# Kernel tuning notes

Measured on AMD Instinct MI355X. Metric: run time of the kernel, lower is better.

## Reference

```python
import jax, jax.numpy as jnp
import numpy as np


def setup_inputs() -> dict:
    key = jax.random.key(0)
    k1, k2 = jax.random.split(key)
    B, T, F, H = 64, 512, 512, 1024
    x = jax.random.normal(k1, (B, T, F), dtype=jnp.float32)
    W = jax.random.normal(k2, (F + H, H), dtype=jnp.float32) * (1.0 / np.sqrt(F + H))
    b = jnp.zeros((H,), dtype=jnp.float32)
    return {"x": x, "W": W, "b": b}


def reference(x, W, b):
    # Vanilla tanh RNN: state_t = tanh([x_t, state_{t-1}] @ W + b); return last state.
    B, T, F = x.shape
    H = b.shape[0]
    Wx, Wh = W[:F], W[F:]  # split weight: input part [F,H], recurrent part [H,H]
    # Precompute input projections for all timesteps in one big GEMM.
    xproj = jnp.einsum('btf,fh->bth', x, Wx) + b  # [B,T,H]

    def step(state, xp_t):
        state = jnp.tanh(xp_t + state @ Wh)
        return state, None

    state0 = jnp.zeros((B, H), dtype=x.dtype)
    final_state, _ = jax.lax.scan(step, state0, jnp.swapaxes(xproj, 0, 1))
    return final_state
```

## Files before the change

kernel.cpp:

```cpp
#include <hip/hip_runtime.h>


typedef _Float16 f16;
typedef _Float16 f16x8 __attribute__((ext_vector_type(8)));
typedef _Float16 f16x4 __attribute__((ext_vector_type(4)));
typedef float f32x4 __attribute__((ext_vector_type(4)));

#define B_  64
#define T_  512
#define F_  512
#define H_  1024

#define XPH_OFF  0ull
#define WXT_OFF  67108864ull
#define WHT_OFF  68157440ull
#define SBUF_OFF 70254592ull
#define BAR_OFF  70516736ull
#define WS_NEED  70518784ull

__global__ __launch_bounds__(256) void k_prep(const float* __restrict__ W,
                                              f16* __restrict__ WxT,
                                              f16* __restrict__ WhT) {
  __shared__ float tile[32][33];
  const int tid = threadIdx.x;
  const int kt = blockIdx.x >> 5;
  const int ht = blockIdx.x & 31;
#pragma unroll
  for (int p = 0; p < 4; ++p) {
    int kr = p * 8 + (tid >> 5);
    tile[kr][tid & 31] = W[(size_t)(kt * 32 + kr) * 1024 + ht * 32 + (tid & 31)];
  }
  __syncthreads();
  const int hl = tid >> 3;
  const int kq = tid & 7;
  f16x4 v;
#pragma unroll
  for (int j = 0; j < 4; ++j) v[j] = (f16)tile[kq * 4 + j][hl];
  const int h = ht * 32 + hl;
  const int kg = kt * 32 + kq * 4;
  if (kg < 512) *(f16x4*)(WxT + (size_t)h * 512 + kg) = v;
  else          *(f16x4*)(WhT + (size_t)h * 1024 + (kg - 512)) = v;
}

__global__ __launch_bounds__(256) void k_xproj(const float* __restrict__ x,
                                               const f16* __restrict__ WxT,
                                               const float* __restrict__ bias,
                                               f16* __restrict__ xph) {
  __shared__ __align__(16) unsigned char Al[65536];
  __shared__ __align__(16) unsigned char Bl[65536];
  const int tid = threadIdx.x;
  const int l = tid & 63, w = tid >> 6;
  const int lane15 = l & 15, sub = l >> 4;
  const int m0 = blockIdx.x * 64;
  const int bidx = m0 >> 9;
  const int t0 = m0 & 511;

  {
    const int r = tid >> 2, qq = tid & 3;
    const float* xs = x + (size_t)(m0 + r) * 512;
#pragma unroll
    for (int i = 0; i < 16; ++i) {
      int s = qq * 16 + i;
      int c = s ^ (r & 7);
      const float4 f0 = *(const float4*)(xs + c * 8);
      const float4 f1 = *(const float4*)(xs + c * 8 + 4);
      f16x8 v;
      v[0] = (f16)f0.x; v[1] = (f16)f0.y; v[2] = (f16)f0.z; v[3] = (f16)f0.w;
      v[4] = (f16)f1.x; v[5] = (f16)f1.y; v[6] = (f16)f1.z; v[7] = (f16)f1.w;
      *(f16x8*)(Al + r * 1024 + s * 16) = v;
    }
  }

  const int mh = (w >> 1) * 32, nh = (w & 1) * 32;
  const int rA0 = mh + lane15, rA1 = mh + 16 + lane15;
  const int rB0 = nh + lane15, rB1 = nh + 16 + lane15;

  for (int nb = 0; nb < 16; ++nb) {
    const int n0 = nb * 64;
    __syncthreads();
    {
      const int r = tid >> 2, qq = tid & 3;
      const f16* bs = WxT + (size_t)(n0 + r) * 512;
#pragma unroll
      for (int i = 0; i < 16; ++i) {
        int s = qq * 16 + i;
        int c = s ^ (r & 7);
        f16x8 v = *(const f16x8*)(bs + c * 8);
        *(f16x8*)(Bl + r * 1024 + s * 16) = v;
      }
    }
    __syncthreads();
    f32x4 acc00 = {0.f,0.f,0.f,0.f}, acc01 = {0.f,0.f,0.f,0.f};
    f32x4 acc10 = {0.f,0.f,0.f,0.f}, acc11 = {0.f,0.f,0.f,0.f};
#pragma unroll
    for (int kk = 0; kk < 16; ++kk) {
      const int s = kk * 4 + sub;
      f16x8 a0 = *(const f16x8*)(Al + rA0 * 1024 + ((s ^ (rA0 & 7)) << 4));
      f16x8 a1 = *(const f16x8*)(Al + rA1 * 1024 + ((s ^ (rA1 & 7)) << 4));
      f16x8 b0 = *(const f16x8*)(Bl + rB0 * 1024 + ((s ^ (rB0 & 7)) << 4));
      f16x8 b1 = *(const f16x8*)(Bl + rB1 * 1024 + ((s ^ (rB1 & 7)) << 4));
      acc00 = __builtin_amdgcn_mfma_f32_16x16x32_f16(a0, b0, acc00, 0, 0, 0);
      acc01 = __builtin_amdgcn_mfma_f32_16x16x32_f16(a0, b1, acc01, 0, 0, 0);
      acc10 = __builtin_amdgcn_mfma_f32_16x16x32_f16(a1, b0, acc10, 0, 0, 0);
      acc11 = __builtin_amdgcn_mfma_f32_16x16x32_f16(a1, b1, acc11, 0, 0, 0);
    }
    const float bv0 = bias[n0 + nh + lane15];
    const float bv1 = bias[n0 + nh + 16 + lane15];
#pragma unroll
    for (int j = 0; j < 4; ++j) {
      const int r0 = mh + sub * 4 + j;
      const int r1 = mh + 16 + sub * 4 + j;
      const size_t row0 = (size_t)(t0 + r0) * 64 + bidx;
      const size_t row1 = (size_t)(t0 + r1) * 64 + bidx;
      xph[row0 * 1024 + n0 + nh + lane15]      = (f16)(acc00[j] + bv0);
      xph[row0 * 1024 + n0 + nh + 16 + lane15] = (f16)(acc01[j] + bv1);
      xph[row1 * 1024 + n0 + nh + lane15]      = (f16)(acc10[j] + bv0);
      xph[row1 * 1024 + n0 + nh + 16 + lane15] = (f16)(acc11[j] + bv1);
    }
  }
}

__global__ __launch_bounds__(256, 1) void k_rnn(const f16* __restrict__ xph,
                                                const f16* __restrict__ WhT,
                                                f16* sbuf, unsigned* bar,
                                                float* __restrict__ out) {
  __shared__ __align__(16) unsigned char lds[32768 + 2176];
  unsigned char* stL  = lds;
  unsigned char* tbuf = lds + 32768;
  const int tid = threadIdx.x;
  const int l = tid & 63, w = tid >> 6;
  const int lane15 = l & 15, sub = l >> 4;
  const int bid = blockIdx.x;
  const int group = (bid & 7) >> 1;
  const int slice = (bid >> 3) * 2 + (bid & 1);

  const int colL = slice * 64 + w * 16 + lane15;
  f16x8 breg[32];
  {
    const f16* src = WhT + (size_t)colL * 1024 + sub * 8;
#pragma unroll
    for (int kk = 0; kk < 32; ++kk) breg[kk] = *(const f16x8*)(src + kk * 32);
  }
  const int rA = lane15, xA = rA & 7;
  const unsigned char* stLb = stL + rA * 2048;

  const int p = tid >> 4, q = tid & 15;
  unsigned* myflag   = bar + (group * 16 + slice) * 8;
  unsigned* pollflag = bar + (group * 16 + p) * 8;
  const bool do_poll = (p != slice);

  for (int t = 0; t < T_; ++t) {
    const char* ib = (const char*)sbuf + (size_t)(t & 1) * 131072 + group * 32768;
    char*       ob = (char*)sbuf + (size_t)((t + 1) & 1) * 131072 + group * 32768;

    float xpv[4];
#pragma unroll
    for (int j = 0; j < 4; ++j)
      xpv[j] = (float)xph[(size_t)(t * 64 + group * 16 + sub * 4 + j) * 1024 + colL];

    if (t > 0 && do_poll) {
      while (__hip_atomic_load(pollflag, __ATOMIC_RELAXED,
                               __HIP_MEMORY_SCOPE_AGENT) < (unsigned)t) {}
    }
    {
      unsigned long long tmp[16];
      const char* src = ib + p * 128 + q * 8;
#pragma unroll
      for (int i = 0; i < 16; ++i)
        tmp[i] = __hip_atomic_load((const unsigned long long*)(src + i * 2048),
                                   __ATOMIC_RELAXED, __HIP_MEMORY_SCOPE_AGENT);
#pragma unroll
      for (int i = 0; i < 16; ++i)
        *(unsigned long long*)(stL + i * 2048 + p * 128 + q * 8) = tmp[i];
    }
    __syncthreads();

    f32x4 acc0 = {0.f,0.f,0.f,0.f}, acc1 = {0.f,0.f,0.f,0.f};
    f32x4 acc2 = {0.f,0.f,0.f,0.f}, acc3 = {0.f,0.f,0.f,0.f};
#pragma unroll
    for (int kk = 0; kk < 32; kk += 4) {
      f16x8 a0 = *(const f16x8*)(stLb + ((((kk + 0) * 4 + sub) ^ xA) << 4));
      f16x8 a1 = *(const f16x8*)(stLb + ((((kk + 1) * 4 + sub) ^ xA) << 4));
      f16x8 a2 = *(const f16x8*)(stLb + ((((kk + 2) * 4 + sub) ^ xA) << 4));
      f16x8 a3 = *(const f16x8*)(stLb + ((((kk + 3) * 4 + sub) ^ xA) << 4));
      acc0 = __builtin_amdgcn_mfma_f32_16x16x32_f16(a0, breg[kk + 0], acc0, 0, 0, 0);
      acc1 = __builtin_amdgcn_mfma_f32_16x16x32_f16(a1, breg[kk + 1], acc1, 0, 0, 0);
      acc2 = __builtin_amdgcn_mfma_f32_16x16x32_f16(a2, breg[kk + 2], acc2, 0, 0, 0);
      acc3 = __builtin_amdgcn_mfma_f32_16x16x32_f16(a3, breg[kk + 3], acc3, 0, 0, 0);
    }
    float rv[4];
#pragma unroll
    for (int j = 0; j < 4; ++j)
      rv[j] = acc0[j] + acc1[j] + acc2[j] + acc3[j] + xpv[j];

    if (t == T_ - 1) {
#pragma unroll
      for (int j = 0; j < 4; ++j)
        out[(size_t)(group * 16 + sub * 4 + j) * 1024 + colL] = tanhf(rv[j]);
      break;
    }

#pragma unroll
    for (int j = 0; j < 4; ++j) {
      f16 hv = (f16)tanhf(rv[j]);
      *(f16*)(tbuf + (sub * 4 + j) * 136 + (w * 16 + lane15) * 2) = hv;
    }
    asm volatile("s_waitcnt lgkmcnt(0)" ::: "memory");
    const int rr = lane15, cg = sub;
    unsigned long long packed =
        *(const unsigned long long*)(tbuf + rr * 136 + (w * 16 + cg * 4) * 2);
    const int c0 = slice * 64 + w * 16 + cg * 4;
    const int byteoff = rr * 2048 + (((c0 >> 3) ^ (rr & 7)) << 4) + (c0 & 7) * 2;
    __hip_atomic_store((unsigned long long*)(ob + byteoff), packed,
                       __ATOMIC_RELAXED, __HIP_MEMORY_SCOPE_AGENT);

    asm volatile("s_waitcnt vmcnt(0)" ::: "memory");
    __syncthreads();
    if (tid == 0)
      __hip_atomic_store(myflag, (unsigned)(t + 1),
                         __ATOMIC_RELAXED, __HIP_MEMORY_SCOPE_AGENT);
  }
}

extern "C" void kernel_launch(void* const* d_in, const int* in_sizes, int n_in,
                              void* d_out, int out_size, void* d_ws, size_t ws_size,
                              hipStream_t stream) {
  const float* x    = (const float*)d_in[0];
  const float* W    = (const float*)d_in[1];
  const float* bias = (const float*)d_in[2];
  float* out = (float*)d_out;
  char* w = (char*)d_ws;

  f16* xph = (f16*)(w + XPH_OFF);
  f16* WxT = (f16*)(w + WXT_OFF);
  f16* WhT = (f16*)(w + WHT_OFF);
  f16* sbuf = (f16*)(w + SBUF_OFF);
  unsigned* bar = (unsigned*)(w + BAR_OFF);

  hipMemsetAsync(w + SBUF_OFF, 0, 262144 + 2048, stream);

  k_prep<<<dim3(48 * 32), dim3(256), 0, stream>>>(W, WxT, WhT);
  k_xproj<<<dim3(512), dim3(256), 0, stream>>>(x, WxT, bias, xph);
  k_rnn<<<dim3(64), dim3(256), 0, stream>>>(xph, WhT, sbuf, bar, out);
}
```

Measured before the change: 1.808 ms.

## Replace flag barrier with per-element step tags in the recurrent state exchange

Each fp16 hidden value is now stored in a 32-bit word together with the step index, so consumers poll the data words themselves instead of waiting on per-slice flags. This removes the vmcnt wait, the extra __syncthreads and the separate flag store and poll that sat on each timestep's critical path. The cost is that the exchanged state doubles in size, and there is extra unpacking and tag-checking work per load. A register pin on the weight fragments is also added.

```diff
diff --git a/kernel.cpp b/kernel.cpp
--- a/kernel.cpp
+++ b/kernel.cpp
@@ -5,6 +5,8 @@
 typedef _Float16 f16x8 __attribute__((ext_vector_type(8)));
 typedef _Float16 f16x4 __attribute__((ext_vector_type(4)));
 typedef float f32x4 __attribute__((ext_vector_type(4)));
+typedef unsigned long long u64;
+typedef unsigned u32;
 
 #define B_  64
 #define T_  512
@@ -15,8 +17,10 @@
 #define WXT_OFF  67108864ull
 #define WHT_OFF  68157440ull
 #define SBUF_OFF 70254592ull
-#define BAR_OFF  70516736ull
-#define WS_NEED  70518784ull
+#define WS_NEED  70778880ull
+
+#define ALD(p)    __hip_atomic_load((const u64*)(p), __ATOMIC_RELAXED, __HIP_MEMORY_SCOPE_AGENT)
+#define AST(p, v) __hip_atomic_store((u64*)(p), (v), __ATOMIC_RELAXED, __HIP_MEMORY_SCOPE_AGENT)
 
 __global__ __launch_bounds__(256) void k_prep(const float* __restrict__ W,
                                               f16* __restrict__ WxT,
@@ -122,9 +126,9 @@
 
 __global__ __launch_bounds__(256, 1) void k_rnn(const f16* __restrict__ xph,
                                                 const f16* __restrict__ WhT,
-                                                f16* sbuf, unsigned* bar,
+                                                u32* sbuf,
                                                 float* __restrict__ out) {
-  __shared__ __align__(16) unsigned char lds[32768 + 2176];
+  __shared__ __align__(16) unsigned char lds[32768 + 4352];
   unsigned char* stL  = lds;
   unsigned char* tbuf = lds + 32768;
   const int tid = threadIdx.x;
@@ -141,37 +145,50 @@
 #pragma unroll
     for (int kk = 0; kk < 32; ++kk) breg[kk] = *(const f16x8*)(src + kk * 32);
   }
+#pragma unroll
+  for (int kk = 0; kk < 32; ++kk) asm volatile("" : "+v"(breg[kk]));
+
   const int rA = lane15, xA = rA & 7;
   const unsigned char* stLb = stL + rA * 2048;
 
   const int p = tid >> 4, q = tid & 15;
-  unsigned* myflag   = bar + (group * 16 + slice) * 8;
-  unsigned* pollflag = bar + (group * 16 + p) * 8;
-  const bool do_poll = (p != slice);
+  const int cg = p * 64 + q * 4;
+  const int ldsoff0 = ((cg >> 3) << 4) + (cg & 7) * 2;
 
   for (int t = 0; t < T_; ++t) {
-    const char* ib = (const char*)sbuf + (size_t)(t & 1) * 131072 + group * 32768;
-    char*       ob = (char*)sbuf + (size_t)((t + 1) & 1) * 131072 + group * 32768;
+    const char* ib = (const char*)sbuf + (size_t)(t & 1) * 262144 + group * 65536;
+    char*       ob = (char*)sbuf + (size_t)((t + 1) & 1) * 262144 + group * 65536;
 
     float xpv[4];
 #pragma unroll
     for (int j = 0; j < 4; ++j)
       xpv[j] = (float)xph[(size_t)(t * 64 + group * 16 + sub * 4 + j) * 1024 + colL];
 
-    if (t > 0 && do_poll) {
-      while (__hip_atomic_load(pollflag, __ATOMIC_RELAXED,
-                               __HIP_MEMORY_SCOPE_AGENT) < (unsigned)t) {}
-    }
-    {
-      unsigned long long tmp[16];
-      const char* src = ib + p * 128 + q * 8;
-#pragma unroll
-      for (int i = 0; i < 16; ++i)
-        tmp[i] = __hip_atomic_load((const unsigned long long*)(src + i * 2048),
-                                   __ATOMIC_RELAXED, __HIP_MEMORY_SCOPE_AGENT);
-#pragma unroll
-      for (int i = 0; i < 16; ++i)
-        *(unsigned long long*)(stL + i * 2048 + p * 128 + q * 8) = tmp[i];
+    u64 v[32];
+    const char* src = ib + p * 256 + q * 16;
+#pragma unroll
+    for (int i = 0; i < 16; ++i) {
+      v[2 * i]     = ALD(src + i * 4096);
+      v[2 * i + 1] = ALD(src + i * 4096 + 8);
+    }
+    const u32 tg = (u32)t;
+    for (;;) {
+      bool all_ok = true;
+#pragma unroll
+      for (int i = 0; i < 32; ++i) {
+        bool ok = ((u32)(v[i] >> 16) & 0xFFFFu) == tg && (u32)(v[i] >> 48) == tg;
+        if (!ok) { all_ok = false; v[i] = ALD(src + (i >> 1) * 4096 + (i & 1) * 8); }
+      }
+      if (all_ok) break;
+    }
+#pragma unroll
+    for (int i = 0; i < 16; ++i) {
+      u64 A = v[2 * i], Bv = v[2 * i + 1];
+      u32 w0 = ((u32)A  & 0xFFFFu) | ((u32)(A  >> 16) & 0xFFFF0000u);
+      u32 w1 = ((u32)Bv & 0xFFFFu) | ((u32)(Bv >> 16) & 0xFFFF0000u);
+      u64 pk = (u64)w0 | ((u64)w1 << 32);
+      const int off = i * 2048 + (ldsoff0 ^ (((i & 7)) << 4));
+      *(u64*)(stL + off) = pk;
     }
     __syncthreads();
 
@@ -203,22 +220,22 @@
 #pragma unroll
     for (int j = 0; j < 4; ++j) {
       f16 hv = (f16)tanhf(rv[j]);
-      *(f16*)(tbuf + (sub * 4 + j) * 136 + (w * 16 + lane15) * 2) = hv;
+      unsigned short bits;
+      __builtin_memcpy(&bits, &hv, 2);
+      u32 wrd = (u32)bits | ((u32)(t + 1) << 16);
+      *(u32*)(tbuf + (sub * 4 + j) * 272 + (w * 16 + lane15) * 4) = wrd;
     }
     asm volatile("s_waitcnt lgkmcnt(0)" ::: "memory");
-    const int rr = lane15, cg = sub;
-    unsigned long long packed =
-        *(const unsigned long long*)(tbuf + rr * 136 + (w * 16 + cg * 4) * 2);
-    const int c0 = slice * 64 + w * 16 + cg * 4;
-    const int byteoff = rr * 2048 + (((c0 >> 3) ^ (rr & 7)) << 4) + (c0 & 7) * 2;
-    __hip_atomic_store((unsigned long long*)(ob + byteoff), packed,
-                       __ATOMIC_RELAXED, __HIP_MEMORY_SCOPE_AGENT);
-
-    asm volatile("s_waitcnt vmcnt(0)" ::: "memory");
-    __syncthreads();
-    if (tid == 0)
-      __hip_atomic_store(myflag, (unsigned)(t + 1),
-                         __ATOMIC_RELAXED, __HIP_MEMORY_SCOPE_AGENT);
+    {
+      const int rr = lane15;
+      const u64* tp = (const u64*)(tbuf + rr * 272 + (w * 16 + sub * 4) * 4);
+      u64 P0 = tp[0], P1 = tp[1];
+      const int c0 = slice * 64 + w * 16 + sub * 4;
+      char* dst = ob + rr * 4096 + c0 * 4;
+      AST(dst, P0);
+      AST(dst + 8, P1);
+    }
+    __syncthreads();
   }
 }
 
@@ -234,12 +251,11 @@
   f16* xph = (f16*)(w + XPH_OFF);
   f16* WxT = (f16*)(w + WXT_OFF);
   f16* WhT = (f16*)(w + WHT_OFF);
-  f16* sbuf = (f16*)(w + SBUF_OFF);
-  unsigned* bar = (unsigned*)(w + BAR_OFF);
-
-  hipMemsetAsync(w + SBUF_OFF, 0, 262144 + 2048, stream);
+  u32* sbuf = (u32*)(w + SBUF_OFF);
+
+  hipMemsetAsync(w + SBUF_OFF, 0, 524288, stream);
 
   k_prep<<<dim3(48 * 32), dim3(256), 0, stream>>>(W, WxT, WhT);
   k_xproj<<<dim3(512), dim3(256), 0, stream>>>(x, WxT, bias, xph);
-  k_rnn<<<dim3(64), dim3(256), 0, stream>>>(xph, WhT, sbuf, bar, out);
-}
+  k_rnn<<<dim3(64), dim3(256), 0, stream>>>(xph, WhT, sbuf, out);
+}
```

Result: slower. 2.862 ms (+58.3%).

## Interleave two batch groups per RNN block to hide cross-block sync latency

Applied to the files above, without the earlier changes.

Each persistent RNN block now handles two batch groups (A and B) with double LDS state buffers and half as many blocks. While one group's MFMA step computes, the other group's flag poll and global state load are issued, so inter-block communication latency overlaps with compute. This costs twice the serial MFMA work per block and per-group flags, and halves the number of CUs used.

```diff
diff --git a/kernel.cpp b/kernel.cpp
--- a/kernel.cpp
+++ b/kernel.cpp
@@ -5,6 +5,8 @@
 typedef _Float16 f16x8 __attribute__((ext_vector_type(8)));
 typedef _Float16 f16x4 __attribute__((ext_vector_type(4)));
 typedef float f32x4 __attribute__((ext_vector_type(4)));
+typedef unsigned long long u64;
+typedef unsigned u32;
 
 #define B_  64
 #define T_  512
@@ -17,6 +19,11 @@
 #define SBUF_OFF 70254592ull
 #define BAR_OFF  70516736ull
 #define WS_NEED  70518784ull
+
+#define ALD64(p)    __hip_atomic_load((const u64*)(p), __ATOMIC_RELAXED, __HIP_MEMORY_SCOPE_AGENT)
+#define AST64(p, v) __hip_atomic_store((u64*)(p), (v), __ATOMIC_RELAXED, __HIP_MEMORY_SCOPE_AGENT)
+#define ALD32(p)    __hip_atomic_load((const u32*)(p), __ATOMIC_RELAXED, __HIP_MEMORY_SCOPE_AGENT)
+#define AST32(p, v) __hip_atomic_store((u32*)(p), (v), __ATOMIC_RELAXED, __HIP_MEMORY_SCOPE_AGENT)
 
 __global__ __launch_bounds__(256) void k_prep(const float* __restrict__ W,
                                               f16* __restrict__ WxT,
@@ -124,15 +131,17 @@
                                                 const f16* __restrict__ WhT,
                                                 f16* sbuf, unsigned* bar,
                                                 float* __restrict__ out) {
-  __shared__ __align__(16) unsigned char lds[32768 + 2176];
-  unsigned char* stL  = lds;
-  unsigned char* tbuf = lds + 32768;
+  __shared__ __align__(16) unsigned char lds[65536 + 2176];
+  unsigned char* stA  = lds;
+  unsigned char* stB  = lds + 32768;
+  unsigned char* tbuf = lds + 65536;
   const int tid = threadIdx.x;
   const int l = tid & 63, w = tid >> 6;
   const int lane15 = l & 15, sub = l >> 4;
   const int bid = blockIdx.x;
-  const int group = (bid & 7) >> 1;
-  const int slice = (bid >> 3) * 2 + (bid & 1);
+  const int pair = bid & 1;
+  const int slice = bid >> 1;
+  const int gA = pair * 2, gB = pair * 2 + 1;
 
   const int colL = slice * 64 + w * 16 + lane15;
   f16x8 breg[32];
@@ -141,84 +150,137 @@
 #pragma unroll
     for (int kk = 0; kk < 32; ++kk) breg[kk] = *(const f16x8*)(src + kk * 32);
   }
+#pragma unroll
+  for (int kk = 0; kk < 32; ++kk) asm volatile("" : "+v"(breg[kk]));
+
   const int rA = lane15, xA = rA & 7;
-  const unsigned char* stLb = stL + rA * 2048;
+  const unsigned char* stAb = stA + rA * 2048;
+  const unsigned char* stBb = stB + rA * 2048;
 
   const int p = tid >> 4, q = tid & 15;
-  unsigned* myflag   = bar + (group * 16 + slice) * 8;
-  unsigned* pollflag = bar + (group * 16 + p) * 8;
-  const bool do_poll = (p != slice);
+  unsigned* flagA = bar + (gA * 16 + slice) * 8;
+  unsigned* flagB = bar + (gB * 16 + slice) * 8;
+  unsigned* pollA = bar + (gA * 16 + p) * 8;
+  unsigned* pollB = bar + (gB * 16 + p) * 8;
+  const size_t baseA = (size_t)gA * 32768;
+  const size_t baseB = (size_t)gB * 32768;
+
+  const int c0s = slice * 64 + w * 16 + sub * 4;
+  const int stoff = lane15 * 2048 + (((c0s >> 3) ^ (lane15 & 7)) << 4) + (c0s & 7) * 2;
+
+#pragma unroll
+  for (int i = 0; i < 16; ++i) *(u64*)(stA + i * 2048 + tid * 8) = 0ull;
+  float xpvA[4], xpvB[4];
+#pragma unroll
+  for (int j = 0; j < 4; ++j)
+    xpvA[j] = (float)xph[(size_t)(gA * 16 + sub * 4 + j) * 1024 + colL];
+  __syncthreads();
 
   for (int t = 0; t < T_; ++t) {
-    const char* ib = (const char*)sbuf + (size_t)(t & 1) * 131072 + group * 32768;
-    char*       ob = (char*)sbuf + (size_t)((t + 1) & 1) * 131072 + group * 32768;
-
-    float xpv[4];
-#pragma unroll
-    for (int j = 0; j < 4; ++j)
-      xpv[j] = (float)xph[(size_t)(t * 64 + group * 16 + sub * 4 + j) * 1024 + colL];
-
-    if (t > 0 && do_poll) {
-      while (__hip_atomic_load(pollflag, __ATOMIC_RELAXED,
-                               __HIP_MEMORY_SCOPE_AGENT) < (unsigned)t) {}
-    }
+    u64 tmp[16];
     {
-      unsigned long long tmp[16];
-      const char* src = ib + p * 128 + q * 8;
+      f32x4 acc0 = {0.f,0.f,0.f,0.f}, acc1 = {0.f,0.f,0.f,0.f};
+      f32x4 acc2 = {0.f,0.f,0.f,0.f}, acc3 = {0.f,0.f,0.f,0.f};
+#pragma unroll
+      for (int kk = 0; kk < 32; kk += 4) {
+        f16x8 a0 = *(const f16x8*)(stAb + ((((kk + 0) * 4 + sub) ^ xA) << 4));
+        f16x8 a1 = *(const f16x8*)(stAb + ((((kk + 1) * 4 + sub) ^ xA) << 4));
+        f16x8 a2 = *(const f16x8*)(stAb + ((((kk + 2) * 4 + sub) ^ xA) << 4));
+        f16x8 a3 = *(const f16x8*)(stAb + ((((kk + 3) * 4 + sub) ^ xA) << 4));
+        acc0 = __builtin_amdgcn_mfma_f32_16x16x32_f16(a0, breg[kk + 0], acc0, 0, 0, 0);
+        acc1 = __builtin_amdgcn_mfma_f32_16x16x32_f16(a1, breg[kk + 1], acc1, 0, 0, 0);
+        acc2 = __builtin_amdgcn_mfma_f32_16x16x32_f16(a2, breg[kk + 2], acc2, 0, 0, 0);
+        acc3 = __builtin_amdgcn_mfma_f32_16x16x32_f16(a3, breg[kk + 3], acc3, 0, 0, 0);
+      }
+#pragma unroll
+      for (int j = 0; j < 4; ++j)
+        xpvB[j] = (float)xph[(size_t)(t * 64 + gB * 16 + sub * 4 + j) * 1024 + colL];
+      if (t > 0) {
+        while (ALD32(pollB) < (u32)t) {}
+      }
+      asm volatile("" ::: "memory");
+      {
+        const char* src = (const char*)sbuf + (size_t)(t & 1) * 131072 + baseB + p * 128 + q * 8;
+#pragma unroll
+        for (int i = 0; i < 16; ++i) tmp[i] = ALD64(src + i * 2048);
+      }
+      float rv[4];
+#pragma unroll
+      for (int j = 0; j < 4; ++j)
+        rv[j] = acc0[j] + acc1[j] + acc2[j] + acc3[j] + xpvA[j];
+      if (t == T_ - 1) {
+#pragma unroll
+        for (int j = 0; j < 4; ++j)
+          out[(size_t)(gA * 16 + sub * 4 + j) * 1024 + colL] = tanhf(rv[j]);
+      } else {
+#pragma unroll
+        for (int j = 0; j < 4; ++j) {
+          f16 hv = (f16)tanhf(rv[j]);
+          *(f16*)(tbuf + (sub * 4 + j) * 136 + (w * 16 + lane15) * 2) = hv;
+        }
+        asm volatile("s_waitcnt lgkmcnt(0)" ::: "memory");
+        u64 packed = *(const u64*)(tbuf + lane15 * 136 + (w * 16 + sub * 4) * 2);
+        char* dst = (char*)sbuf + (size_t)((t + 1) & 1) * 131072 + baseA + stoff;
+        AST64(dst, packed);
+      }
+      asm volatile("s_waitcnt vmcnt(0)" ::: "memory");
 #pragma unroll
       for (int i = 0; i < 16; ++i)
-        tmp[i] = __hip_atomic_load((const unsigned long long*)(src + i * 2048),
-                                   __ATOMIC_RELAXED, __HIP_MEMORY_SCOPE_AGENT);
+        *(u64*)(stB + i * 2048 + p * 128 + q * 8) = tmp[i];
+      __syncthreads();
+      if (t < T_ - 1 && tid == 0) AST32(flagA, (u32)(t + 1));
+    }
+
+    {
+      f32x4 acc0 = {0.f,0.f,0.f,0.f}, acc1 = {0.f,0.f,0.f,0.f};
+      f32x4 acc2 = {0.f,0.f,0.f,0.f}, acc3 = {0.f,0.f,0.f,0.f};
+#pragma unroll
+      for (int kk = 0; kk < 32; kk += 4) {
+        f16x8 a0 = *(const f16x8*)(stBb + ((((kk + 0) * 4 + sub) ^ xA) << 4));
+        f16x8 a1 = *(const f16x8*)(stBb + ((((kk + 1) * 4 + sub) ^ xA) << 4));
+        f16x8 a2 = *(const f16x8*)(stBb + ((((kk + 2) * 4 + sub) ^ xA) << 4));
+        f16x8 a3 = *(const f16x8*)(stBb + ((((kk + 3) * 4 + sub) ^ xA) << 4));
+        acc0 = __builtin_amdgcn_mfma_f32_16x16x32_f16(a0, breg[kk + 0], acc0, 0, 0, 0);
+        acc1 = __builtin_amdgcn_mfma_f32_16x16x32_f16(a1, breg[kk + 1], acc1, 0, 0, 0);
+        acc2 = __builtin_amdgcn_mfma_f32_16x16x32_f16(a2, breg[kk + 2], acc2, 0, 0, 0);
+        acc3 = __builtin_amdgcn_mfma_f32_16x16x32_f16(a3, breg[kk + 3], acc3, 0, 0, 0);
+      }
+      if (t < T_ - 1) {
+#pragma unroll
+        for (int j = 0; j < 4; ++j)
+          xpvA[j] = (float)xph[(size_t)((t + 1) * 64 + gA * 16 + sub * 4 + j) * 1024 + colL];
+        while (ALD32(pollA) < (u32)(t + 1)) {}
+        asm volatile("" ::: "memory");
+        const char* src = (const char*)sbuf + (size_t)((t + 1) & 1) * 131072 + baseA + p * 128 + q * 8;
+#pragma unroll
+        for (int i = 0; i < 16; ++i) tmp[i] = ALD64(src + i * 2048);
+      }
+      float rv[4];
+#pragma unroll
+      for (int j = 0; j < 4; ++j)
+        rv[j] = acc0[j] + acc1[j] + acc2[j] + acc3[j] + xpvB[j];
+      if (t == T_ - 1) {
+#pragma unroll
+        for (int j = 0; j < 4; ++j)
+          out[(size_t)(gB * 16 + sub * 4 + j) * 1024 + colL] = tanhf(rv[j]);
+        break;
+      }
+#pragma unroll
+      for (int j = 0; j < 4; ++j) {
+        f16 hv = (f16)tanhf(rv[j]);
+        *(f16*)(tbuf + (sub * 4 + j) * 136 + (w * 16 + lane15) * 2) = hv;
+      }
+      asm volatile("s_waitcnt lgkmcnt(0)" ::: "memory");
+      u64 packed = *(const u64*)(tbuf + lane15 * 136 + (w * 16 + sub * 4) * 2);
+      char* dst = (char*)sbuf + (size_t)((t + 1) & 1) * 131072 + baseB + stoff;
+      AST64(dst, packed);
+      asm volatile("s_waitcnt vmcnt(0)" ::: "memory");
 #pragma unroll
       for (int i = 0; i < 16; ++i)
-        *(unsigned long long*)(stL + i * 2048 + p * 128 + q * 8) = tmp[i];
-    }
-    __syncthreads();
-
-    f32x4 acc0 = {0.f,0.f,0.f,0.f}, acc1 = {0.f,0.f,0.f,0.f};
-    f32x4 acc2 = {0.f,0.f,0.f,0.f}, acc3 = {0.f,0.f,0.f,0.f};
-#pragma unroll
-    for (int kk = 0; kk < 32; kk += 4) {
-      f16x8 a0 = *(const f16x8*)(stLb + ((((kk + 0) * 4 + sub) ^ xA) << 4));
-      f16x8 a1 = *(const f16x8*)(stLb + ((((kk + 1) * 4 + sub) ^ xA) << 4));
-      f16x8 a2 = *(const f16x8*)(stLb + ((((kk + 2) * 4 + sub) ^ xA) << 4));
-      f16x8 a3 = *(const f16x8*)(stLb + ((((kk + 3) * 4 + sub) ^ xA) << 4));
-      acc0 = __builtin_amdgcn_mfma_f32_16x16x32_f16(a0, breg[kk + 0], acc0, 0, 0, 0);
-      acc1 = __builtin_amdgcn_mfma_f32_16x16x32_f16(a1, breg[kk + 1], acc1, 0, 0, 0);
-      acc2 = __builtin_amdgcn_mfma_f32_16x16x32_f16(a2, breg[kk + 2], acc2, 0, 0, 0);
-      acc3 = __builtin_amdgcn_mfma_f32_16x16x32_f16(a3, breg[kk + 3], acc3, 0, 0, 0);
-    }
-    float rv[4];
-#pragma unroll
-    for (int j = 0; j < 4; ++j)
-      rv[j] = acc0[j] + acc1[j] + acc2[j] + acc3[j] + xpv[j];
-
-    if (t == T_ - 1) {
-#pragma unroll
-      for (int j = 0; j < 4; ++j)
-        out[(size_t)(group * 16 + sub * 4 + j) * 1024 + colL] = tanhf(rv[j]);
-      break;
-    }
-
-#pragma unroll
-    for (int j = 0; j < 4; ++j) {
-      f16 hv = (f16)tanhf(rv[j]);
-      *(f16*)(tbuf + (sub * 4 + j) * 136 + (w * 16 + lane15) * 2) = hv;
-    }
-    asm volatile("s_waitcnt lgkmcnt(0)" ::: "memory");
-    const int rr = lane15, cg = sub;
-    unsigned long long packed =
-        *(const unsigned long long*)(tbuf + rr * 136 + (w * 16 + cg * 4) * 2);
-    const int c0 = slice * 64 + w * 16 + cg * 4;
-    const int byteoff = rr * 2048 + (((c0 >> 3) ^ (rr & 7)) << 4) + (c0 & 7) * 2;
-    __hip_atomic_store((unsigned long long*)(ob + byteoff), packed,
-                       __ATOMIC_RELAXED, __HIP_MEMORY_SCOPE_AGENT);
-
-    asm volatile("s_waitcnt vmcnt(0)" ::: "memory");
-    __syncthreads();
-    if (tid == 0)
-      __hip_atomic_store(myflag, (unsigned)(t + 1),
-                         __ATOMIC_RELAXED, __HIP_MEMORY_SCOPE_AGENT);
+        *(u64*)(stA + i * 2048 + p * 128 + q * 8) = tmp[i];
+      __syncthreads();
+      if (tid == 0) AST32(flagB, (u32)(t + 1));
+    }
   }
 }
 
@@ -241,5 +303,5 @@
 
   k_prep<<<dim3(48 * 32), dim3(256), 0, stream>>>(W, WxT, WhT);
   k_xproj<<<dim3(512), dim3(256), 0, stream>>>(x, WxT, bias, xph);
-  k_rnn<<<dim3(64), dim3(256), 0, stream>>>(xph, WhT, sbuf, bar, out);
+  k_rnn<<<dim3(32), dim3(256), 0, stream>>>(xph, WhT, sbuf, bar, out);
 }
```

New measurement: 2.497 ms. +38.1%, slower.

## Load recurrent state fragments directly from global and use per-wave flags

Applied to the files above, without the earlier changes.

The per-step staging of the shared hidden state through LDS is removed. Each wave now loads its MFMA A-fragments straight from the global state buffer with atomic 64-bit loads, writes the state unswizzled, and raises its own completion flag per wave. The block-wide __syncthreads and single-thread flag publish are replaced by a wave-wide poll over 64 flags, and the block-to-group mapping changes. This cuts barrier latency and LDS traffic on the serial critical path, at the cost of more global load instructions per step and much higher register pressure.

```diff
diff --git a/kernel.cpp b/kernel.cpp
--- a/kernel.cpp
+++ b/kernel.cpp
@@ -5,6 +5,9 @@
 typedef _Float16 f16x8 __attribute__((ext_vector_type(8)));
 typedef _Float16 f16x4 __attribute__((ext_vector_type(4)));
 typedef float f32x4 __attribute__((ext_vector_type(4)));
+typedef unsigned long long u64;
+typedef unsigned u32;
+typedef unsigned long long u64x2 __attribute__((ext_vector_type(2)));
 
 #define B_  64
 #define T_  512
@@ -17,6 +20,11 @@
 #define SBUF_OFF 70254592ull
 #define BAR_OFF  70516736ull
 #define WS_NEED  70518784ull
+
+#define ALD64(p)    __hip_atomic_load((const u64*)(p), __ATOMIC_RELAXED, __HIP_MEMORY_SCOPE_AGENT)
+#define AST64(p, v) __hip_atomic_store((u64*)(p), (v), __ATOMIC_RELAXED, __HIP_MEMORY_SCOPE_AGENT)
+#define ALD32(p)    __hip_atomic_load((const u32*)(p), __ATOMIC_RELAXED, __HIP_MEMORY_SCOPE_AGENT)
+#define AST32(p, v) __hip_atomic_store((u32*)(p), (v), __ATOMIC_RELAXED, __HIP_MEMORY_SCOPE_AGENT)
 
 __global__ __launch_bounds__(256) void k_prep(const float* __restrict__ W,
                                               f16* __restrict__ WxT,
@@ -124,15 +132,13 @@
                                                 const f16* __restrict__ WhT,
                                                 f16* sbuf, unsigned* bar,
                                                 float* __restrict__ out) {
-  __shared__ __align__(16) unsigned char lds[32768 + 2176];
-  unsigned char* stL  = lds;
-  unsigned char* tbuf = lds + 32768;
+  __shared__ __align__(16) unsigned char tbuf[2176];
   const int tid = threadIdx.x;
   const int l = tid & 63, w = tid >> 6;
   const int lane15 = l & 15, sub = l >> 4;
   const int bid = blockIdx.x;
-  const int group = (bid & 7) >> 1;
-  const int slice = (bid >> 3) * 2 + (bid & 1);
+  const int group = bid & 3;
+  const int slice = bid >> 2;
 
   const int colL = slice * 64 + w * 16 + lane15;
   f16x8 breg[32];
@@ -141,52 +147,58 @@
 #pragma unroll
     for (int kk = 0; kk < 32; ++kk) breg[kk] = *(const f16x8*)(src + kk * 32);
   }
-  const int rA = lane15, xA = rA & 7;
-  const unsigned char* stLb = stL + rA * 2048;
-
-  const int p = tid >> 4, q = tid & 15;
-  unsigned* myflag   = bar + (group * 16 + slice) * 8;
-  unsigned* pollflag = bar + (group * 16 + p) * 8;
-  const bool do_poll = (p != slice);
+#pragma unroll
+  for (int kk = 0; kk < 32; ++kk) asm volatile("" : "+v"(breg[kk]));
+
+  unsigned* gflags = bar + group * 128;
+  unsigned* myflag = gflags + (slice * 4 + w);
+  unsigned* pollp  = gflags + l;
+  const size_t gbase = (size_t)group * 32768;
+
+  const int fragoff = lane15 * 2048 + sub * 16;
+  const int c0 = slice * 64 + w * 16 + sub * 4;
+  const int stoff = lane15 * 2048 + c0 * 2;
 
   for (int t = 0; t < T_; ++t) {
-    const char* ib = (const char*)sbuf + (size_t)(t & 1) * 131072 + group * 32768;
-    char*       ob = (char*)sbuf + (size_t)((t + 1) & 1) * 131072 + group * 32768;
+    const char* ib = (const char*)sbuf + (size_t)(t & 1) * 131072 + gbase;
+    char*       ob = (char*)sbuf + (size_t)((t + 1) & 1) * 131072 + gbase;
 
     float xpv[4];
 #pragma unroll
     for (int j = 0; j < 4; ++j)
       xpv[j] = (float)xph[(size_t)(t * 64 + group * 16 + sub * 4 + j) * 1024 + colL];
 
-    if (t > 0 && do_poll) {
-      while (__hip_atomic_load(pollflag, __ATOMIC_RELAXED,
-                               __HIP_MEMORY_SCOPE_AGENT) < (unsigned)t) {}
-    }
+    if (t > 0) {
+      u32 fv = ALD32(pollp);
+      while (!__all((int)(fv >= (u32)t))) fv = ALD32(pollp);
+    }
+    asm volatile("" ::: "memory");
+
+    u64 flo[32], fhi[32];
     {
-      unsigned long long tmp[16];
-      const char* src = ib + p * 128 + q * 8;
-#pragma unroll
-      for (int i = 0; i < 16; ++i)
-        tmp[i] = __hip_atomic_load((const unsigned long long*)(src + i * 2048),
-                                   __ATOMIC_RELAXED, __HIP_MEMORY_SCOPE_AGENT);
-#pragma unroll
-      for (int i = 0; i < 16; ++i)
-        *(unsigned long long*)(stL + i * 2048 + p * 128 + q * 8) = tmp[i];
-    }
-    __syncthreads();
-
+      const char* rb = ib + fragoff;
+#pragma unroll
+      for (int kk = 0; kk < 32; ++kk) {
+        flo[kk] = ALD64(rb + kk * 64);
+        fhi[kk] = ALD64(rb + kk * 64 + 8);
+      }
+    }
     f32x4 acc0 = {0.f,0.f,0.f,0.f}, acc1 = {0.f,0.f,0.f,0.f};
     f32x4 acc2 = {0.f,0.f,0.f,0.f}, acc3 = {0.f,0.f,0.f,0.f};
 #pragma unroll
     for (int kk = 0; kk < 32; kk += 4) {
-      f16x8 a0 = *(const f16x8*)(stLb + ((((kk + 0) * 4 + sub) ^ xA) << 4));
-      f16x8 a1 = *(const f16x8*)(stLb + ((((kk + 1) * 4 + sub) ^ xA) << 4));
-      f16x8 a2 = *(const f16x8*)(stLb + ((((kk + 2) * 4 + sub) ^ xA) << 4));
-      f16x8 a3 = *(const f16x8*)(stLb + ((((kk + 3) * 4 + sub) ^ xA) << 4));
-      acc0 = __builtin_amdgcn_mfma_f32_16x16x32_f16(a0, breg[kk + 0], acc0, 0, 0, 0);
-      acc1 = __builtin_amdgcn_mfma_f32_16x16x32_f16(a1, breg[kk + 1], acc1, 0, 0, 0);
-      acc2 = __builtin_amdgcn_mfma_f32_16x16x32_f16(a2, breg[kk + 2], acc2, 0, 0, 0);
-      acc3 = __builtin_amdgcn_mfma_f32_16x16x32_f16(a3, breg[kk + 3], acc3, 0, 0, 0);
+      u64x2 p0; p0[0] = flo[kk + 0]; p0[1] = fhi[kk + 0];
+      u64x2 p1; p1[0] = flo[kk + 1]; p1[1] = fhi[kk + 1];
+      u64x2 p2; p2[0] = flo[kk + 2]; p2[1] = fhi[kk + 2];
+      u64x2 p3; p3[0] = flo[kk + 3]; p3[1] = fhi[kk + 3];
+      acc0 = __builtin_amdgcn_mfma_f32_16x16x32_f16(
+          __builtin_bit_cast(f16x8, p0), breg[kk + 0], acc0, 0, 0, 0);
+      acc1 = __builtin_amdgcn_mfma_f32_16x16x32_f16(
+          __builtin_bit_cast(f16x8, p1), breg[kk + 1], acc1, 0, 0, 0);
+      acc2 = __builtin_amdgcn_mfma_f32_16x16x32_f16(
+          __builtin_bit_cast(f16x8, p2), breg[kk + 2], acc2, 0, 0, 0);
+      acc3 = __builtin_amdgcn_mfma_f32_16x16x32_f16(
+          __builtin_bit_cast(f16x8, p3), breg[kk + 3], acc3, 0, 0, 0);
     }
     float rv[4];
 #pragma unroll
@@ -206,19 +218,12 @@
       *(f16*)(tbuf + (sub * 4 + j) * 136 + (w * 16 + lane15) * 2) = hv;
     }
     asm volatile("s_waitcnt lgkmcnt(0)" ::: "memory");
-    const int rr = lane15, cg = sub;
-    unsigned long long packed =
-        *(const unsigned long long*)(tbuf + rr * 136 + (w * 16 + cg * 4) * 2);
-    const int c0 = slice * 64 + w * 16 + cg * 4;
-    const int byteoff = rr * 2048 + (((c0 >> 3) ^ (rr & 7)) << 4) + (c0 & 7) * 2;
-    __hip_atomic_store((unsigned long long*)(ob + byteoff), packed,
-                       __ATOMIC_RELAXED, __HIP_MEMORY_SCOPE_AGENT);
-
+    {
+      u64 packed = *(const u64*)(tbuf + lane15 * 136 + (w * 16 + sub * 4) * 2);
+      AST64(ob + stoff, packed);
+    }
     asm volatile("s_waitcnt vmcnt(0)" ::: "memory");
-    __syncthreads();
-    if (tid == 0)
-      __hip_atomic_store(myflag, (unsigned)(t + 1),
-                         __ATOMIC_RELAXED, __HIP_MEMORY_SCOPE_AGENT);
+    if (l == 0) AST32(myflag, (u32)(t + 1));
   }
 }
 
```

Result: slower. 5.906 ms (+226.7%).
